# Kernel optimization log

Hardware: AMD Instinct MI355X
Metric: run time of the kernel (lower is better)

## Reference

```python
import jax, jax.numpy as jnp
import numpy as np


def setup_inputs() -> dict:
    key = jax.random.key(0)
    k1, k2 = jax.random.split(key)
    B, S, D_IN, D_OUT = 4, 8192, 768, 768
    x = jax.random.normal(k1, (B, S, D_IN), dtype=jnp.float32)
    # kaiming_normal_(mode='fan_out', nonlinearity='linear') -> std = 1/sqrt(fan_out)
    weight = jax.random.normal(k2, (D_OUT, D_IN), dtype=jnp.float32) * (1.0 / jnp.sqrt(D_OUT))
    return {"x": x, "weight": weight}


def reference(x, weight):
    # Binarize weights with sign (0 -> 0, matching torch.sign), then F.linear:
    # out[..., o] = sum_i x[..., i] * sign(W)[o, i]
    w_bin = jnp.sign(weight)
    return jnp.einsum('bsi,oi->bso', x, w_bin)
```

## Files before the change

### kernel.cpp

```cpp
#include <hip/hip_runtime.h>
#include <hip/hip_bf16.h>

using f32x4 = __attribute__((ext_vector_type(4))) float;
using s16x8 = __attribute__((ext_vector_type(8))) short;

constexpr int KDIM = 768;
constexpr int NDIM = 768;
constexpr int BM = 128;
constexpr int BN = 128;
constexpr int BK = 32;
constexpr int NBN = NDIM / BN;
constexpr int NT = KDIM / BK;

__device__ __forceinline__ unsigned short f2bf(float f) {
    __bf16 h = (__bf16)f;
    return __builtin_bit_cast(unsigned short, h);
}

__device__ __forceinline__ short sgnbf(float w) {
    unsigned u = __builtin_bit_cast(unsigned, w);
    return (w != 0.f) ? (short)(unsigned short)(0x3F80u | ((u >> 16) & 0x8000u))
                      : (short)0;
}

__device__ __forceinline__ s16x8 cvt8(float4 u, float4 v) {
    s16x8 c;
    c[0] = (short)f2bf(u.x); c[1] = (short)f2bf(u.y);
    c[2] = (short)f2bf(u.z); c[3] = (short)f2bf(u.w);
    c[4] = (short)f2bf(v.x); c[5] = (short)f2bf(v.y);
    c[6] = (short)f2bf(v.z); c[7] = (short)f2bf(v.w);
    return c;
}

__global__ void binarize_w(const float* __restrict__ W, unsigned short* __restrict__ Wf) {
    const int g = blockIdx.x * 256 + threadIdx.x;
    const int lane = g & 63;
    const int grp  = g >> 6;
    const int n16l = grp & 7;
    const int bkt  = grp >> 3;
    const int bn   = bkt % NBN;
    const int kt   = bkt / NBN;
    const int col  = bn * 128 + n16l * 16 + (lane & 15);
    const int k0   = kt * 32 + (lane >> 4) * 8;
    const float* src = W + (size_t)col * KDIM + k0;
    s16x8 r;
    #pragma unroll
    for (int j = 0; j < 8; ++j) r[j] = sgnbf(src[j]);
    *(s16x8*)(Wf + (size_t)g * 8) = r;
}

#define BAR_NODRAIN() do {                                        \
    asm volatile("s_waitcnt lgkmcnt(0)" ::: "memory");            \
    __builtin_amdgcn_s_barrier();                                 \
    asm volatile("" ::: "memory");                                \
} while (0)

template<bool PRE>
__global__ __launch_bounds__(256, 3)
void binlin_mfma(const float* __restrict__ X, const float* __restrict__ W,
                 const unsigned short* __restrict__ Wf, float* __restrict__ Out) {
    __shared__ __align__(16) unsigned short As[2][512 * 8];
    __shared__ __align__(16) unsigned short Bs[2][512 * 8];

    const int bid = blockIdx.x;
    const int cpx = gridDim.x >> 3;
    const int swz = (bid & 7) * cpx + (bid >> 3);
    const int bm = swz / NBN;
    const int bn = swz - bm * NBN;

    const int t    = threadIdx.x;
    const int lane = t & 63;
    const int wid  = t >> 6;
    const int wm   = (wid >> 1) * 64;
    const int wn   = (wid & 1) * 64;
    const int wm16 = (wid >> 1) * 4;
    const int wn16 = (wid & 1) * 4;

    const float* Xb = X + (size_t)bm * BM * KDIM;

    const int r   = t >> 2;
    const int c8  = (t & 3) * 8;
    const float* Abase = Xb + (size_t)r * KDIM + c8;
    const int sA1 = (r >> 4) * 64 + (r & 15) + 16 * (t & 3);
    const int sA2 = sA1 + 256;

    auto loadA = [&](int kt, float4 a[4]) {
        const float* p = Abase + kt * BK;
        a[0] = *(const float4*)p;
        a[1] = *(const float4*)(p + 4);
        a[2] = *(const float4*)(p + (size_t)64 * KDIM);
        a[3] = *(const float4*)(p + (size_t)64 * KDIM + 4);
    };
    auto writeA = [&](int buf, float4 a[4]) {
        *(s16x8*)&As[buf][(size_t)sA1 * 8] = cvt8(a[0], a[1]);
        *(s16x8*)&As[buf][(size_t)sA2 * 8] = cvt8(a[2], a[3]);
    };
    auto loadB = [&](int kt, s16x8 b[2]) {
        if constexpr (PRE) {
            const unsigned short* q = Wf + ((size_t)(kt * NBN + bn) * 512 + 2 * t) * 8;
            b[0] = *(const s16x8*)q;
            b[1] = *(const s16x8*)(q + 8);
        } else {
            #pragma unroll
            for (int i = 0; i < 2; ++i) {
                const int s    = 2 * t + i;
                const int col  = bn * 128 + (s >> 6) * 16 + (s & 15);
                const int k0   = kt * 32 + ((s >> 4) & 3) * 8;
                const float* wp = W + (size_t)col * KDIM + k0;
                float4 u = *(const float4*)wp;
                float4 v = *(const float4*)(wp + 4);
                s16x8 c;
                c[0] = sgnbf(u.x); c[1] = sgnbf(u.y); c[2] = sgnbf(u.z); c[3] = sgnbf(u.w);
                c[4] = sgnbf(v.x); c[5] = sgnbf(v.y); c[6] = sgnbf(v.z); c[7] = sgnbf(v.w);
                b[i] = c;
            }
        }
    };
    auto writeB = [&](int buf, s16x8 b[2]) {
        *(s16x8*)&Bs[buf][(size_t)(2 * t) * 8]     = b[0];
        *(s16x8*)&Bs[buf][(size_t)(2 * t + 1) * 8] = b[1];
    };

    f32x4 acc[4][4] = {};
    float4 A0[4], A1[4];
    s16x8  B0[2], B1[2];

    loadA(0, A0); loadB(0, B0);
    loadA(1, A1); loadB(1, B1);
    writeA(0, A0); writeB(0, B0);
    BAR_NODRAIN();

    #pragma unroll
    for (int kt = 0; kt < NT; ++kt) {
        const int c = kt & 1;
        float4 (&AFree)[4] = c ? A1 : A0;
        float4 (&AWr)[4]   = c ? A0 : A1;
        s16x8  (&BFree)[2] = c ? B1 : B0;
        s16x8  (&BWr)[2]   = c ? B0 : B1;

        if (kt + 2 < NT) { loadA(kt + 2, AFree); loadB(kt + 2, BFree); }

        s16x8 af[4], bf_[4];
        #pragma unroll
        for (int m = 0; m < 4; ++m)
            af[m] = *(const s16x8*)&As[c][(size_t)((wm16 + m) * 64 + lane) * 8];
        #pragma unroll
        for (int n = 0; n < 4; ++n)
            bf_[n] = *(const s16x8*)&Bs[c][(size_t)((wn16 + n) * 64 + lane) * 8];

        #pragma unroll
        for (int m = 0; m < 4; ++m)
            #pragma unroll
            for (int n = 0; n < 4; ++n)
                acc[m][n] = __builtin_amdgcn_mfma_f32_16x16x32_bf16(
                    af[m], bf_[n], acc[m][n], 0, 0, 0);

        if (kt + 1 < NT) {
            writeA(c ^ 1, AWr); writeB(c ^ 1, BWr);
            BAR_NODRAIN();
        }
    }

    float* Ob = Out + (size_t)(bm * BM) * NDIM + bn * BN;
    const int lr = lane & 15;
    #pragma unroll
    for (int m = 0; m < 4; ++m) {
        const int row0 = wm + m * 16 + (lane >> 4) * 4;
        #pragma unroll
        for (int n = 0; n < 4; ++n) {
            const int col = wn + n * 16 + lr;
            #pragma unroll
            for (int rr = 0; rr < 4; ++rr)
                Ob[(size_t)(row0 + rr) * NDIM + col] = acc[m][n][rr];
        }
    }
}

extern "C" void kernel_launch(void* const* d_in, const int* in_sizes, int n_in,
                              void* d_out, int out_size, void* d_ws, size_t ws_size,
                              hipStream_t stream) {
    const float* X = (const float*)d_in[0];
    const float* W = (const float*)d_in[1];
    float* Out = (float*)d_out;
    const int M = in_sizes[0] / KDIM;
    const int grid = (M / BM) * NBN;
    const size_t need = (size_t)NDIM * KDIM * sizeof(unsigned short);

    if (ws_size >= need) {
        unsigned short* Wf = (unsigned short*)d_ws;
        binarize_w<<<(NT * NBN * 8 * 64) / 256, 256, 0, stream>>>(W, Wf);
        binlin_mfma<true><<<grid, 256, 0, stream>>>(X, W, Wf, Out);
    } else {
        binlin_mfma<false><<<grid, 256, 0, stream>>>(X, W, nullptr, Out);
    }
}
```

Before: 60.91 us.

## Stream binarized weight tiles straight into LDS with a 4-stage buffer

The precomputed binarized weight tiles now go from global memory directly into shared memory through global_load_lds. This replaces the global-load, register, LDS-store round trip, and B tiles are prefetched three iterations ahead using four LDS buffers. Scheduling barriers keep the fragment reads and prefetch issues apart from the MFMA block, and the fallback path is simplified to single-stage register prefetch. The aim is lower VGPR pressure and fewer LDS write instructions on the weight path, at the cost of more LDS per block. The barrier waits only on lgkmcnt, not vmcnt, so correctness of the DMA data depends on ordering implied by the A-load waits.

```diff
diff --git a/kernel.cpp b/kernel.cpp
--- a/kernel.cpp
+++ b/kernel.cpp
@@ -49,18 +49,21 @@
     *(s16x8*)(Wf + (size_t)g * 8) = r;
 }
 
-#define BAR_NODRAIN() do {                                        \
-    asm volatile("s_waitcnt lgkmcnt(0)" ::: "memory");            \
-    __builtin_amdgcn_s_barrier();                                 \
-    asm volatile("" ::: "memory");                                \
-} while (0)
+#define SCHED_FENCE() __builtin_amdgcn_sched_barrier(0)
+
+__device__ __forceinline__ void gload_lds16(const void* g, void* l) {
+    __builtin_amdgcn_global_load_lds(
+        (const __attribute__((address_space(1))) unsigned int*)g,
+        (__attribute__((address_space(3))) unsigned int*)l,
+        16, 0, 0);
+}
 
 template<bool PRE>
 __global__ __launch_bounds__(256, 3)
 void binlin_mfma(const float* __restrict__ X, const float* __restrict__ W,
                  const unsigned short* __restrict__ Wf, float* __restrict__ Out) {
     __shared__ __align__(16) unsigned short As[2][512 * 8];
-    __shared__ __align__(16) unsigned short Bs[2][512 * 8];
+    __shared__ __align__(16) unsigned short Bs[4][512 * 8];
 
     const int bid = blockIdx.x;
     const int cpx = gridDim.x >> 3;
@@ -79,8 +82,7 @@
     const float* Xb = X + (size_t)bm * BM * KDIM;
 
     const int r   = t >> 2;
-    const int c8  = (t & 3) * 8;
-    const float* Abase = Xb + (size_t)r * KDIM + c8;
+    const float* Abase = Xb + (size_t)r * KDIM + (t & 3) * 8;
     const int sA1 = (r >> 4) * 64 + (r & 15) + 16 * (t & 3);
     const int sA2 = sA1 + 256;
 
@@ -95,69 +97,103 @@
         *(s16x8*)&As[buf][(size_t)sA1 * 8] = cvt8(a[0], a[1]);
         *(s16x8*)&As[buf][(size_t)sA2 * 8] = cvt8(a[2], a[3]);
     };
-    auto loadB = [&](int kt, s16x8 b[2]) {
-        if constexpr (PRE) {
-            const unsigned short* q = Wf + ((size_t)(kt * NBN + bn) * 512 + 2 * t) * 8;
-            b[0] = *(const s16x8*)q;
-            b[1] = *(const s16x8*)(q + 8);
-        } else {
-            #pragma unroll
-            for (int i = 0; i < 2; ++i) {
-                const int s    = 2 * t + i;
-                const int col  = bn * 128 + (s >> 6) * 16 + (s & 15);
-                const int k0   = kt * 32 + ((s >> 4) & 3) * 8;
-                const float* wp = W + (size_t)col * KDIM + k0;
-                float4 u = *(const float4*)wp;
-                float4 v = *(const float4*)(wp + 4);
-                s16x8 c;
-                c[0] = sgnbf(u.x); c[1] = sgnbf(u.y); c[2] = sgnbf(u.z); c[3] = sgnbf(u.w);
-                c[4] = sgnbf(v.x); c[5] = sgnbf(v.y); c[6] = sgnbf(v.z); c[7] = sgnbf(v.w);
-                b[i] = c;
-            }
-        }
-    };
-    auto writeB = [&](int buf, s16x8 b[2]) {
-        *(s16x8*)&Bs[buf][(size_t)(2 * t) * 8]     = b[0];
-        *(s16x8*)&Bs[buf][(size_t)(2 * t + 1) * 8] = b[1];
+    auto dmaB = [&](int buf, int kt) {
+        const unsigned short* chunk = Wf + (size_t)(kt * NBN + bn) * 512 * 8;
+        #pragma unroll
+        for (int i = 0; i < 2; ++i) {
+            const int slotbase = (i * 4 + wid) * 64;
+            gload_lds16(chunk + (size_t)(slotbase + lane) * 8,
+                        &Bs[buf][(size_t)slotbase * 8]);
+        }
+    };
+    auto stageB_reg = [&](int buf, int kt) {
+        #pragma unroll
+        for (int i = 0; i < 2; ++i) {
+            const int s   = 2 * t + i;
+            const int col = bn * 128 + (s >> 6) * 16 + (s & 15);
+            const int k0  = kt * 32 + ((s >> 4) & 3) * 8;
+            const float* wp = W + (size_t)col * KDIM + k0;
+            float4 u = *(const float4*)wp;
+            float4 v = *(const float4*)(wp + 4);
+            s16x8 c;
+            c[0] = sgnbf(u.x); c[1] = sgnbf(u.y); c[2] = sgnbf(u.z); c[3] = sgnbf(u.w);
+            c[4] = sgnbf(v.x); c[5] = sgnbf(v.y); c[6] = sgnbf(v.z); c[7] = sgnbf(v.w);
+            *(s16x8*)&Bs[buf][(size_t)s * 8] = c;
+        }
     };
 
     f32x4 acc[4][4] = {};
     float4 A0[4], A1[4];
-    s16x8  B0[2], B1[2];
-
-    loadA(0, A0); loadB(0, B0);
-    loadA(1, A1); loadB(1, B1);
-    writeA(0, A0); writeB(0, B0);
-    BAR_NODRAIN();
-
-    #pragma unroll
-    for (int kt = 0; kt < NT; ++kt) {
-        const int c = kt & 1;
-        float4 (&AFree)[4] = c ? A1 : A0;
-        float4 (&AWr)[4]   = c ? A0 : A1;
-        s16x8  (&BFree)[2] = c ? B1 : B0;
-        s16x8  (&BWr)[2]   = c ? B0 : B1;
-
-        if (kt + 2 < NT) { loadA(kt + 2, AFree); loadB(kt + 2, BFree); }
-
-        s16x8 af[4], bf_[4];
-        #pragma unroll
-        for (int m = 0; m < 4; ++m)
-            af[m] = *(const s16x8*)&As[c][(size_t)((wm16 + m) * 64 + lane) * 8];
-        #pragma unroll
-        for (int n = 0; n < 4; ++n)
-            bf_[n] = *(const s16x8*)&Bs[c][(size_t)((wn16 + n) * 64 + lane) * 8];
-
-        #pragma unroll
-        for (int m = 0; m < 4; ++m)
+
+    if constexpr (PRE) {
+        dmaB(0, 0); dmaB(1, 1); dmaB(2, 2);
+        loadA(0, A0);
+        loadA(1, A1);
+        writeA(0, A0);
+        asm volatile("s_waitcnt lgkmcnt(0)" ::: "memory");
+        __builtin_amdgcn_s_barrier();
+        asm volatile("" ::: "memory");
+
+        #pragma unroll
+        for (int kt = 0; kt < NT; ++kt) {
+            float4 (&AL)[4] = (kt & 1) ? A1 : A0;
+            float4 (&AW)[4] = (kt & 1) ? A0 : A1;
+
+            s16x8 af[4], bf_[4];
+            #pragma unroll
+            for (int m = 0; m < 4; ++m)
+                af[m] = *(const s16x8*)&As[kt & 1][(size_t)((wm16 + m) * 64 + lane) * 8];
             #pragma unroll
             for (int n = 0; n < 4; ++n)
-                acc[m][n] = __builtin_amdgcn_mfma_f32_16x16x32_bf16(
-                    af[m], bf_[n], acc[m][n], 0, 0, 0);
-
-        if (kt + 1 < NT) {
-            writeA(c ^ 1, AWr); writeB(c ^ 1, BWr);
-            BAR_NODRAIN();
+                bf_[n] = *(const s16x8*)&Bs[kt & 3][(size_t)((wn16 + n) * 64 + lane) * 8];
+
+            if (kt + 2 < NT) loadA(kt + 2, AL);
+            if (kt + 3 < NT) dmaB((kt + 3) & 3, kt + 3);
+            SCHED_FENCE();
+
+            #pragma unroll
+            for (int m = 0; m < 4; ++m)
+                #pragma unroll
+                for (int n = 0; n < 4; ++n)
+                    acc[m][n] = __builtin_amdgcn_mfma_f32_16x16x32_bf16(
+                        af[m], bf_[n], acc[m][n], 0, 0, 0);
+
+            SCHED_FENCE();
+            if (kt + 1 < NT) writeA((kt + 1) & 1, AW);
+            asm volatile("s_waitcnt lgkmcnt(0)" ::: "memory");
+            __builtin_amdgcn_s_barrier();
+            asm volatile("" ::: "memory");
+        }
+    } else {
+        float4 aR[4]; s16x8 bR0[2];
+        loadA(0, aR);
+        writeA(0, aR);
+        stageB_reg(0, 0);
+        __syncthreads();
+        #pragma unroll 2
+        for (int kt = 0; kt < NT; ++kt) {
+            const int c = kt & 1;
+            const bool pf = (kt + 1 < NT);
+            if (pf) loadA(kt + 1, aR);
+            s16x8 af[4], bf_[4];
+            #pragma unroll
+            for (int m = 0; m < 4; ++m)
+                af[m] = *(const s16x8*)&As[c][(size_t)((wm16 + m) * 64 + lane) * 8];
+            #pragma unroll
+            for (int n = 0; n < 4; ++n)
+                bf_[n] = *(const s16x8*)&Bs[c][(size_t)((wn16 + n) * 64 + lane) * 8];
+            #pragma unroll
+            for (int m = 0; m < 4; ++m)
+                #pragma unroll
+                for (int n = 0; n < 4; ++n)
+                    acc[m][n] = __builtin_amdgcn_mfma_f32_16x16x32_bf16(
+                        af[m], bf_[n], acc[m][n], 0, 0, 0);
+            if (pf) {
+                writeA(c ^ 1, aR);
+                stageB_reg(c ^ 1, kt + 1);
+            }
+            __syncthreads();
+            (void)bR0;
         }
     }
 
```

Measured after the change: 72.97 us. 19.8% more time.
